# Performance work log

Measured on AMD Instinct MI355X. Metric: run time of the kernel, lower is better.

Reference implementation:

```python
import jax, jax.numpy as jnp
import numpy as np

B, S, E, H, T = 2, 1024, 1024, 16, 32
D = E // H  # head_dim = 64
EPS = 1e-12
SCALE = float(np.sqrt(T) / np.sqrt(D))  # sqrt(num_templates) * 1/sqrt(head_dim)


def _apply_rope(q, k):
    # q, k: [B, S, H, D] float32 (source casts to float for RoPE)
    d = q.shape[-1]
    s = q.shape[1]
    inv_freq = 1.0 / (10000.0 ** (jnp.arange(0, d, 2, dtype=jnp.float32) / d))
    ang = jnp.arange(s, dtype=jnp.float32)[:, None] * inv_freq[None, :]  # [S, D/2]
    cis = jnp.exp(1j * ang)[None, :, None, :]  # [1, S, 1, D/2] complex64

    def rot(v):
        vc = v.reshape(v.shape[:-1] + (d // 2, 2))
        vc = jax.lax.complex(vc[..., 0], vc[..., 1]) * cis
        return jnp.stack([jnp.real(vc), jnp.imag(vc)], axis=-1).reshape(v.shape)

    return rot(q), rot(k)


def _l2norm(v):
    # F.normalize(v, dim=-1): v / max(||v||, eps)
    n = jnp.sqrt(jnp.sum(v * v, axis=-1, keepdims=True))
    return v / jnp.maximum(n, EPS)


def _forward(x, Wq, Wk, Wv, Wo, templates, bind_proj):
    b, s, e = x.shape
    h, d = H, D
    q = (x @ Wq.T).reshape(b, s, h, d)
    k = (x @ Wk.T).reshape(b, s, h, d)
    v = (x @ Wv.T).reshape(b, s, h, d)
    q, k = _apply_rope(q, k)
    q = q.transpose(0, 2, 1, 3)  # [B,H,S,D]
    k = k.transpose(0, 2, 1, 3)
    v = v.transpose(0, 2, 1, 3)

    tpl = _l2norm(templates)  # [H,T,D]
    # forward rfft uses norm='ortho' in the source
    q_freq = jnp.fft.rfft(q, axis=-1, norm='ortho')  # [B,H,S,F], F=D//2+1
    k_freq = jnp.fft.rfft(k, axis=-1, norm='ortho')
    t_conj = jnp.conj(jnp.fft.rfft(tpl, axis=-1, norm='ortho'))[None, :, None, :, :]  # [1,H,1,T,F]

    # NOTE: irfft in the source uses the DEFAULT 'backward' norm (asymmetric with
    # the ortho rfft) -- reproduce that exactly.
    q_bind = jnp.fft.irfft(q_freq[:, :, :, None, :] * t_conj, n=d, axis=-1)  # [B,H,S,T,D]
    k_bind = jnp.fft.irfft(k_freq[:, :, :, None, :] * t_conj, n=d, axis=-1)

    proj = bind_proj[None, :, None, None, :]  # [1,H,1,1,D]
    q_sig = _l2norm(jnp.sum(q_bind * proj, axis=-1))  # [B,H,S,T]
    k_sig = _l2norm(jnp.sum(k_bind * proj, axis=-1))

    scores = jnp.einsum('bhqt,bhkt->bhqk', q_sig, k_sig) * SCALE  # [B,H,S,S]
    attn = jax.nn.softmax(scores, axis=-1)  # dropout is identity in eval mode
    out = jnp.einsum('bhqk,bhkd->bqhd', attn, v).reshape(b, s, e)
    return out @ Wo.T


def setup_inputs() -> dict:
    key = jax.random.key(0)
    ks = jax.random.split(key, 7)
    lim = 1.0 / np.sqrt(E)
    x = jax.random.normal(ks[0], (B, S, E), jnp.float32)
    Wq = jax.random.uniform(ks[1], (E, E), jnp.float32, -lim, lim)
    Wk = jax.random.uniform(ks[2], (E, E), jnp.float32, -lim, lim)
    Wv = jax.random.uniform(ks[3], (E, E), jnp.float32, -lim, lim)
    Wo = jax.random.uniform(ks[4], (E, E), jnp.float32, -lim, lim)
    templates = jax.random.normal(ks[5], (H, T, D), jnp.float32)
    bind_proj = jax.random.normal(ks[6], (H, D), jnp.float32) * 0.02
    return {"x": x, "Wq": Wq, "Wk": Wk, "Wv": Wv, "Wo": Wo,
            "templates": templates, "bind_proj": bind_proj}


def reference(x, Wq, Wk, Wv, Wo, templates, bind_proj):
    return _forward(x, Wq, Wk, Wv, Wo, templates, bind_proj)
```

## Files before the change

kernel.cpp:

```cpp
#include <hip/hip_runtime.h>
#include <math.h>

#define S_ 1024
#define T_ 32
#define SCALE_F 0.7071067811865476f

typedef unsigned int uint;
typedef unsigned short ushort;
typedef __bf16 bf16x8 __attribute__((ext_vector_type(8)));
typedef float f32x16 __attribute__((ext_vector_type(16)));

union FragU { uint4 q; bf16x8 v; };

#define MFMA(a, b, c) __builtin_amdgcn_mfma_f32_32x32x16_bf16((a), (b), (c), 0, 0, 0)

__device__ __forceinline__ uint rne16(float f) {
  uint u = __builtin_bit_cast(uint, f);
  u += 0x7fffu + ((u >> 16) & 1u);
  return u >> 16;
}

__device__ __forceinline__ void split8a(const float* f, uint4& hi, uint4& lo) {
  uint h[8], m[8];
#pragma unroll
  for (int i = 0; i < 8; ++i) {
    uint u = __builtin_bit_cast(uint, f[i]);
    h[i] = u >> 16;
    float fh = __builtin_bit_cast(float, u & 0xffff0000u);
    m[i] = __builtin_bit_cast(uint, f[i] - fh) >> 16;
  }
  hi = make_uint4(h[0] | (h[1] << 16), h[2] | (h[3] << 16),
                  h[4] | (h[5] << 16), h[6] | (h[7] << 16));
  lo = make_uint4(m[0] | (m[1] << 16), m[2] | (m[3] << 16),
                  m[4] | (m[5] << 16), m[6] | (m[7] << 16));
}

__device__ __forceinline__ uint4 rne8(const float4& A, const float4& B) {
  float f[8] = {A.x, A.y, A.z, A.w, B.x, B.y, B.z, B.w};
  uint h[8];
#pragma unroll
  for (int i = 0; i < 8; ++i) h[i] = rne16(f[i]);
  return make_uint4(h[0] | (h[1] << 16), h[2] | (h[3] << 16),
                    h[4] | (h[5] << 16), h[6] | (h[7] << 16));
}

__global__ __launch_bounds__(256) void k_cvtall(
    const float* __restrict__ X, const float* __restrict__ Wq,
    const float* __restrict__ Wk, const float* __restrict__ Wv,
    const float* __restrict__ Wo, ushort* __restrict__ Xb,
    ushort* __restrict__ Wqb, ushort* __restrict__ Wkb,
    ushort* __restrict__ Wvb, ushort* __restrict__ Wob) {
  int i = blockIdx.x * 256 + threadIdx.x;
  const float* src;
  ushort* dst;
  int j;
  if (i < 262144)      { src = X;  dst = Xb;  j = i; }
  else if (i < 393216) { src = Wq; dst = Wqb; j = i - 262144; }
  else if (i < 524288) { src = Wk; dst = Wkb; j = i - 393216; }
  else if (i < 655360) { src = Wv; dst = Wvb; j = i - 524288; }
  else                 { src = Wo; dst = Wob; j = i - 655360; }
  float4 a = *reinterpret_cast<const float4*>(src + j * 8);
  float4 b = *reinterpret_cast<const float4*>(src + j * 8 + 4);
  *reinterpret_cast<uint4*>(dst + j * 8) = rne8(a, b);
}

__global__ __launch_bounds__(64) void k_cs(float* __restrict__ cs) {
  int s = blockIdx.x * 2 + (threadIdx.x >> 5);
  int p = threadIdx.x & 31;
  float invf = powf(10000.0f, (-2.0f * p) / 64.0f);
  float sn, c;
  sincosf((float)s * invf, &sn, &c);
  cs[s * 64 + 2 * p] = c;
  cs[s * 64 + 2 * p + 1] = sn;
}

__global__ __launch_bounds__(64) void k_prep_A(const float* __restrict__ tpl,
                                               const float* __restrict__ proj,
                                               ushort* __restrict__ Ahh,
                                               ushort* __restrict__ Ahl) {
  int ht = blockIdx.x;
  int h = ht >> 5;
  int lane = threadIdx.x;
  float tv = tpl[ht * 64 + lane];
  float ss = tv * tv;
#pragma unroll
  for (int off = 1; off < 64; off <<= 1) ss += __shfl_xor(ss, off);
  float rn = 1.0f / fmaxf(sqrtf(ss), 1e-12f);
  __shared__ float tn[64];
  tn[lane] = tv * rn;
  __syncthreads();
  float acc = 0.f;
#pragma unroll
  for (int j = 0; j < 64; ++j) acc += proj[h * 64 + j] * tn[(lane - j) & 63];
  float v = acc * 0.125f;
  uint u = __builtin_bit_cast(uint, v);
  uint hi = u >> 16;
  float fh = __builtin_bit_cast(float, u & 0xffff0000u);
  uint lo = __builtin_bit_cast(uint, v - fh) >> 16;
  Ahh[ht * 64 + lane] = (ushort)hi;
  Ahl[ht * 64 + lane] = (ushort)lo;
}

__global__ __launch_bounds__(256) void k_qkv(
    const ushort* __restrict__ Xb,
    const ushort* __restrict__ Wqb, const ushort* __restrict__ Wkb,
    const ushort* __restrict__ Wvb,
    const ushort* __restrict__ Ahh, const ushort* __restrict__ Ahl,
    const float* __restrict__ cs,
    ushort* __restrict__ Qs, ushort* __restrict__ Ks,
    ushort* __restrict__ Vt) {
  __shared__ __align__(16) char smem[34816];

  const int z = blockIdx.z;
  const ushort* Wm = (z == 0) ? Wqb : (z == 1) ? Wkb : Wvb;
  const int m0 = blockIdx.y * 128;
  const int n0 = blockIdx.x * 64;
  const int h = blockIdx.x;

  const int tid = threadIdx.x;
  const int l = tid & 63;
  const int wid = tid >> 6;
  const int wr = wid >> 1, wc = wid & 1;
  const int l31 = l & 31, lhi = l >> 5;

  const int sr = tid >> 2;
  const int sc = tid & 3;

  const int offA0 = (sr) * 64 + ((sc ^ ((sr >> 1) & 3)) << 4);
  const int offA1 = (sr + 64) * 64 + ((sc ^ (((sr + 64) >> 1) & 3)) << 4);
  const int offB = 8192 + sr * 64 + ((sc ^ ((sr >> 1) & 3)) << 4);

  const ushort* apsrc0 = Xb + (size_t)(m0 + sr) * 1024 + sc * 8;
  const ushort* apsrc1 = Xb + (size_t)(m0 + sr + 64) * 1024 + sc * 8;
  const ushort* bpsrc = Wm + (size_t)(n0 + sr) * 1024 + sc * 8;

  f32x16 acc0 = 0.0f, acc1 = 0.0f;

  {
    uint4 a0 = *reinterpret_cast<const uint4*>(apsrc0);
    uint4 a1 = *reinterpret_cast<const uint4*>(apsrc1);
    uint4 b = *reinterpret_cast<const uint4*>(bpsrc);
    *reinterpret_cast<uint4*>(smem + offA0) = a0;
    *reinterpret_cast<uint4*>(smem + offA1) = a1;
    *reinterpret_cast<uint4*>(smem + offB) = b;
  }
  __syncthreads();

  int cur = 0;
  for (int t = 0; t < 32; ++t) {
    const bool more = (t < 31);
    uint4 na0, na1, nb;
    if (more) {
      const int kn = (t + 1) * 32;
      na0 = *reinterpret_cast<const uint4*>(apsrc0 + kn);
      na1 = *reinterpret_cast<const uint4*>(apsrc1 + kn);
      nb = *reinterpret_cast<const uint4*>(bpsrc + kn);
    }

    const char* base = smem + cur * 12288;
#pragma unroll
    for (int kst = 0; kst < 2; ++kst) {
      FragU ah0, ah1, bh;
      {
        int row = wr * 64 + l31;
        int cc = (kst * 2 + lhi) ^ ((row >> 1) & 3);
        ah0.q = *reinterpret_cast<const uint4*>(base + row * 64 + cc * 16);
      }
      {
        int row = wr * 64 + 32 + l31;
        int cc = (kst * 2 + lhi) ^ ((row >> 1) & 3);
        ah1.q = *reinterpret_cast<const uint4*>(base + row * 64 + cc * 16);
      }
      {
        int brow = wc * 32 + l31;
        int bcc = (kst * 2 + lhi) ^ ((brow >> 1) & 3);
        bh.q = *reinterpret_cast<const uint4*>(base + 8192 + brow * 64 + bcc * 16);
      }
      acc0 = MFMA(ah0.v, bh.v, acc0);
      acc1 = MFMA(ah1.v, bh.v, acc1);
    }

    if (more) {
      char* dst = smem + (cur ^ 1) * 12288;
      *reinterpret_cast<uint4*>(dst + offA0) = na0;
      *reinterpret_cast<uint4*>(dst + offA1) = na1;
      *reinterpret_cast<uint4*>(dst + offB) = nb;
      __syncthreads();
      cur ^= 1;
    }
  }

  if (z == 2) {
    int d = wc * 32 + l31;
#pragma unroll
    for (int fm = 0; fm < 2; ++fm) {
      const f32x16& a = fm ? acc1 : acc0;
#pragma unroll
      for (int j = 0; j < 16; ++j) {
        int rl = fm * 32 + (j & 3) + ((j >> 2) & 3) * 8 + 4 * lhi;
        int m = m0 + wr * 64 + rl;
        int b = m >> 10, s = m & 1023;
        Vt[((size_t)((b * 16 + h) * 64 + d)) * 1024 + s] = (ushort)rne16(a[j]);
      }
    }
    return;
  }

  ushort* Sig = (z == 0) ? Qs : Ks;
  float* dmp = reinterpret_cast<float*>(smem);
  __syncthreads();
#pragma unroll
  for (int fm = 0; fm < 2; ++fm) {
    const f32x16& a = fm ? acc1 : acc0;
#pragma unroll
    for (int j = 0; j < 16; ++j) {
      int rl = fm * 32 + (j & 3) + ((j >> 2) & 3) * 8 + 4 * lhi;
      dmp[(wr * 64 + rl) * 68 + wc * 32 + l31] = a[j];
    }
  }
  __syncthreads();

  int srow = wr * 64 + wc * 32 + l31;
  int sq = (m0 + srow) & 1023;
  f32x16 sacc = 0.0f;
#pragma unroll
  for (int kst = 0; kst < 4; ++kst) {
    const float* dp = &dmp[srow * 68 + kst * 16 + lhi * 8];
    float4 x0 = *reinterpret_cast<const float4*>(dp);
    float4 x1 = *reinterpret_cast<const float4*>(dp + 4);
    const float* cp = &cs[sq * 64 + kst * 16 + lhi * 8];
    float4 c0 = *reinterpret_cast<const float4*>(cp);
    float4 c1 = *reinterpret_cast<const float4*>(cp + 4);
    float r[8];
    r[0] = x0.x * c0.x - x0.y * c0.y;
    r[1] = x0.x * c0.y + x0.y * c0.x;
    r[2] = x0.z * c0.z - x0.w * c0.w;
    r[3] = x0.z * c0.w + x0.w * c0.z;
    r[4] = x1.x * c1.x - x1.y * c1.y;
    r[5] = x1.x * c1.y + x1.y * c1.x;
    r[6] = x1.z * c1.z - x1.w * c1.w;
    r[7] = x1.z * c1.w + x1.w * c1.z;
    FragU ah, al;
    split8a(r, ah.q, al.q);
    size_t boff = ((size_t)(h * 32 + l31) * 64 + kst * 16 + lhi * 8);
    FragU bh, bl;
    bh.q = *reinterpret_cast<const uint4*>(Ahh + boff);
    bl.q = *reinterpret_cast<const uint4*>(Ahl + boff);
    sacc = MFMA(al.v, bh.v, sacc);
    sacc = MFMA(ah.v, bl.v, sacc);
    sacc = MFMA(ah.v, bh.v, sacc);
  }
#pragma unroll
  for (int j = 0; j < 16; ++j) {
    float v = sacc[j];
    float ss = v * v;
    ss += __shfl_xor(ss, 1);
    ss += __shfl_xor(ss, 2);
    ss += __shfl_xor(ss, 4);
    ss += __shfl_xor(ss, 8);
    ss += __shfl_xor(ss, 16);
    float rn = 1.0f / fmaxf(sqrtf(ss), 1e-12f);
    int rl = (j & 3) + ((j >> 2) & 3) * 8 + 4 * lhi;
    int m = m0 + wr * 64 + wc * 32 + rl;
    int bb = m >> 10, s2 = m & 1023;
    Sig[(((size_t)(bb * 16 + h)) * 1024 + s2) * 32 + l31] =
        (ushort)rne16(v * rn);
  }
}

__global__ __launch_bounds__(128) void k_attn(const ushort* __restrict__ Qs,
                                              const ushort* __restrict__ Ks,
                                              const ushort* __restrict__ Vt,
                                              float* __restrict__ Po,
                                              float* __restrict__ Pd) {
  __shared__ ushort plds[2][32][68];

  const int tid = threadIdx.x;
  const int l = tid & 63;
  const int wid = tid >> 6;
  const int l31 = l & 31, lhi = l >> 5;
  const int bh = blockIdx.y;
  const int z = blockIdx.z;
  const int q0 = blockIdx.x * 64 + wid * 32;

  FragU aq0, aq1;
  {
    const ushort* qp = Qs + ((size_t)bh * 1024 + q0 + l31) * 32 + lhi * 8;
    aq0.q = *reinterpret_cast<const uint4*>(qp);
    aq1.q = *reinterpret_cast<const uint4*>(qp + 16);
  }

  const ushort* kbase = Ks + (size_t)bh * 1024 * 32;
  const ushort* vbase = Vt + (size_t)bh * 64 * 1024;

  f32x16 oacc0 = 0.0f, oacc1 = 0.0f;
  float pden[16];
#pragma unroll
  for (int r = 0; r < 16; ++r) pden[r] = 0.f;

  for (int kt = z * 4; kt < z * 4 + 4; ++kt) {
    const int k0 = kt * 64;
    f32x16 sacc[2];
    sacc[0] = 0.0f;
    sacc[1] = 0.0f;
#pragma unroll
    for (int nt = 0; nt < 2; ++nt) {
      const ushort* kp = kbase + (size_t)(k0 + nt * 32 + l31) * 32 + lhi * 8;
      FragU b0, b1;
      b0.q = *reinterpret_cast<const uint4*>(kp);
      b1.q = *reinterpret_cast<const uint4*>(kp + 16);
      sacc[nt] = MFMA(aq0.v, b0.v, sacc[nt]);
      sacc[nt] = MFMA(aq1.v, b1.v, sacc[nt]);
    }
#pragma unroll
    for (int nt = 0; nt < 2; ++nt) {
#pragma unroll
      for (int r = 0; r < 16; ++r) {
        float e = __expf(sacc[nt][r] * SCALE_F);
        pden[r] += e;
        int q = (r & 3) + ((r >> 2) << 3) + 4 * lhi;
        plds[wid][q][nt * 32 + l31] = (ushort)rne16(e);
      }
    }
    __builtin_amdgcn_wave_barrier();
#pragma unroll
    for (int kst = 0; kst < 4; ++kst) {
      FragU ap;
      const ushort* pp = &plds[wid][l31][kst * 16 + lhi * 8];
      uint2 plo = *reinterpret_cast<const uint2*>(pp);
      uint2 phi = *reinterpret_cast<const uint2*>(pp + 4);
      ap.q = make_uint4(plo.x, plo.y, phi.x, phi.y);
      FragU bv0, bv1;
      const ushort* vp0 = vbase + (size_t)l31 * 1024 + k0 + kst * 16 + lhi * 8;
      bv0.q = *reinterpret_cast<const uint4*>(vp0);
      bv1.q = *reinterpret_cast<const uint4*>(vp0 + 32 * 1024);
      oacc0 = MFMA(ap.v, bv0.v, oacc0);
      oacc1 = MFMA(ap.v, bv1.v, oacc1);
    }
  }

#pragma unroll
  for (int r = 0; r < 16; ++r) {
    float s = pden[r];
    s += __shfl_xor(s, 1);
    s += __shfl_xor(s, 2);
    s += __shfl_xor(s, 4);
    s += __shfl_xor(s, 8);
    s += __shfl_xor(s, 16);
    pden[r] = s;
  }

  const size_t zb = (size_t)z * 32 + bh;
#pragma unroll
  for (int r = 0; r < 16; ++r) {
    int q = q0 + (r & 3) + ((r >> 2) << 3) + 4 * lhi;
    size_t row = zb * 1024 + q;
    Po[row * 64 + l31] = oacc0[r];
    Po[row * 64 + 32 + l31] = oacc1[r];
    if (l31 == 0) Pd[row] = pden[r];
  }
}

__global__ __launch_bounds__(256) void k_attnred(const float* __restrict__ Po,
                                                 const float* __restrict__ Pd,
                                                 ushort* __restrict__ O) {
  int idx = blockIdx.x * 4 + (threadIdx.x >> 6);
  int d = threadIdx.x & 63;
  float den = 0.f, val = 0.f;
#pragma unroll
  for (int zc = 0; zc < 4; ++zc) {
    size_t row = (size_t)zc * 32768 + idx;
    den += Pd[row];
    val += Po[row * 64 + d];
  }
  int bh = idx >> 10, q = idx & 1023;
  int b = bh >> 4, h = bh & 15;
  O[((size_t)(b * 1024 + q)) * 1024 + h * 64 + d] = (ushort)rne16(val / den);
}

__global__ __launch_bounds__(128) void k_attn_mono(const ushort* __restrict__ Qs,
                                                   const ushort* __restrict__ Ks,
                                                   const ushort* __restrict__ Vt,
                                                   ushort* __restrict__ O) {
  __shared__ ushort plds[2][32][68];

  const int tid = threadIdx.x;
  const int l = tid & 63;
  const int wid = tid >> 6;
  const int l31 = l & 31, lhi = l >> 5;
  const int bh = blockIdx.y;
  const int q0 = blockIdx.x * 64 + wid * 32;

  FragU aq0, aq1;
  {
    const ushort* qp = Qs + ((size_t)bh * 1024 + q0 + l31) * 32 + lhi * 8;
    aq0.q = *reinterpret_cast<const uint4*>(qp);
    aq1.q = *reinterpret_cast<const uint4*>(qp + 16);
  }

  const ushort* kbase = Ks + (size_t)bh * 1024 * 32;
  const ushort* vbase = Vt + (size_t)bh * 64 * 1024;

  f32x16 oacc0 = 0.0f, oacc1 = 0.0f;
  float pden[16];
#pragma unroll
  for (int r = 0; r < 16; ++r) pden[r] = 0.f;

  for (int kt = 0; kt < 16; ++kt) {
    const int k0 = kt * 64;
    f32x16 sacc[2];
    sacc[0] = 0.0f;
    sacc[1] = 0.0f;
#pragma unroll
    for (int nt = 0; nt < 2; ++nt) {
      const ushort* kp = kbase + (size_t)(k0 + nt * 32 + l31) * 32 + lhi * 8;
      FragU b0, b1;
      b0.q = *reinterpret_cast<const uint4*>(kp);
      b1.q = *reinterpret_cast<const uint4*>(kp + 16);
      sacc[nt] = MFMA(aq0.v, b0.v, sacc[nt]);
      sacc[nt] = MFMA(aq1.v, b1.v, sacc[nt]);
    }
#pragma unroll
    for (int nt = 0; nt < 2; ++nt) {
#pragma unroll
      for (int r = 0; r < 16; ++r) {
        float e = __expf(sacc[nt][r] * SCALE_F);
        pden[r] += e;
        int q = (r & 3) + ((r >> 2) << 3) + 4 * lhi;
        plds[wid][q][nt * 32 + l31] = (ushort)rne16(e);
      }
    }
    __builtin_amdgcn_wave_barrier();
#pragma unroll
    for (int kst = 0; kst < 4; ++kst) {
      FragU ap;
      const ushort* pp = &plds[wid][l31][kst * 16 + lhi * 8];
      uint2 plo = *reinterpret_cast<const uint2*>(pp);
      uint2 phi = *reinterpret_cast<const uint2*>(pp + 4);
      ap.q = make_uint4(plo.x, plo.y, phi.x, phi.y);
      FragU bv0, bv1;
      const ushort* vp0 = vbase + (size_t)l31 * 1024 + k0 + kst * 16 + lhi * 8;
      bv0.q = *reinterpret_cast<const uint4*>(vp0);
      bv1.q = *reinterpret_cast<const uint4*>(vp0 + 32 * 1024);
      oacc0 = MFMA(ap.v, bv0.v, oacc0);
      oacc1 = MFMA(ap.v, bv1.v, oacc1);
    }
  }

#pragma unroll
  for (int r = 0; r < 16; ++r) {
    float s = pden[r];
    s += __shfl_xor(s, 1);
    s += __shfl_xor(s, 2);
    s += __shfl_xor(s, 4);
    s += __shfl_xor(s, 8);
    s += __shfl_xor(s, 16);
    pden[r] = 1.0f / s;
  }

  const int b = bh >> 4, h = bh & 15;
#pragma unroll
  for (int r = 0; r < 16; ++r) {
    int q = q0 + (r & 3) + ((r >> 2) << 3) + 4 * lhi;
    size_t row = ((size_t)b * 1024 + q) * 1024 + h * 64;
    O[row + l31] = (ushort)rne16(oacc0[r] * pden[r]);
    O[row + 32 + l31] = (ushort)rne16(oacc1[r] * pden[r]);
  }
}

__global__ __launch_bounds__(256) void k_final(const ushort* __restrict__ Xb,
                                               const ushort* __restrict__ Wb,
                                               float* __restrict__ Y) {
  __shared__ __align__(16) char smem[16384];

  const int m0 = blockIdx.y * 64;
  const int n0 = blockIdx.x * 64;
  const int tid = threadIdx.x;
  const int l = tid & 63;
  const int wid = tid >> 6;
  const int wr = wid >> 1, wc = wid & 1;
  const int l31 = l & 31, lhi = l >> 5;
  const int sr = tid >> 2;
  const int sc = tid & 3;

  const int offA = sr * 64 + ((sc ^ ((sr >> 1) & 3)) << 4);
  const int offB = 4096 + offA;
  const ushort* apsrc = Xb + (size_t)(m0 + sr) * 1024 + sc * 8;
  const ushort* bpsrc = Wb + (size_t)(n0 + sr) * 1024 + sc * 8;

  f32x16 acc = 0.0f;

  {
    uint4 av = *reinterpret_cast<const uint4*>(apsrc);
    uint4 bv = *reinterpret_cast<const uint4*>(bpsrc);
    *reinterpret_cast<uint4*>(smem + offA) = av;
    *reinterpret_cast<uint4*>(smem + offB) = bv;
  }
  __syncthreads();

  int cur = 0;
  for (int t = 0; t < 32; ++t) {
    const bool more = (t < 31);
    uint4 na, nb;
    if (more) {
      const int kn = (t + 1) * 32;
      na = *reinterpret_cast<const uint4*>(apsrc + kn);
      nb = *reinterpret_cast<const uint4*>(bpsrc + kn);
    }

    const char* base = smem + cur * 8192;
#pragma unroll
    for (int kst = 0; kst < 2; ++kst) {
      FragU ah, bh;
      int row = wr * 32 + l31;
      int cc = (kst * 2 + lhi) ^ ((row >> 1) & 3);
      ah.q = *reinterpret_cast<const uint4*>(base + row * 64 + cc * 16);
      int brow = wc * 32 + l31;
      int bcc = (kst * 2 + lhi) ^ ((brow >> 1) & 3);
      bh.q = *reinterpret_cast<const uint4*>(base + 4096 + brow * 64 + bcc * 16);
      acc = MFMA(ah.v, bh.v, acc);
    }

    if (more) {
      char* dst = smem + (cur ^ 1) * 8192;
      *reinterpret_cast<uint4*>(dst + offA) = na;
      *reinterpret_cast<uint4*>(dst + offB) = nb;
      __syncthreads();
      cur ^= 1;
    }
  }

#pragma unroll
  for (int j = 0; j < 16; ++j) {
    int rl = (j & 3) + ((j >> 2) & 3) * 8 + 4 * lhi;
    int m = m0 + wr * 32 + rl;
    Y[(size_t)m * 1024 + n0 + wc * 32 + l31] = acc[j];
  }
}

extern "C" void kernel_launch(void* const* d_in, const int* in_sizes, int n_in,
                              void* d_out, int out_size, void* d_ws,
                              size_t ws_size, hipStream_t stream) {
  const float* x = (const float*)d_in[0];
  const float* Wq = (const float*)d_in[1];
  const float* Wk = (const float*)d_in[2];
  const float* Wv = (const float*)d_in[3];
  const float* Wo = (const float*)d_in[4];
  const float* tpl = (const float*)d_in[5];
  const float* proj = (const float*)d_in[6];
  float* out = (float*)d_out;

  char* ws = (char*)d_ws;
  size_t off = 0;
  auto alloc = [&](size_t bytes) {
    void* p = ws + off;
    off += (bytes + 255) & ~(size_t)255;
    return p;
  };

  const size_t MB = 1024 * 1024;
  bool huge = ws_size >= 64 * MB;
  bool big = ws_size >= 22 * MB;

  ushort *Xb, *Wvb, *obuf;
  float* cs;
  ushort *Ahh, *Ahl, *Wqb, *Wkb, *Wob, *qs, *ks, *vt;
  float *Po = nullptr, *Pd = nullptr;

  if (big || huge) {
    Xb = (ushort*)alloc(4 * MB);
    cs = (float*)alloc((size_t)1024 * 64 * 4);
    Ahh = (ushort*)alloc((size_t)16 * 32 * 64 * 2);
    Ahl = (ushort*)alloc((size_t)16 * 32 * 64 * 2);
    Wqb = (ushort*)alloc(2 * MB);
    Wkb = (ushort*)alloc(2 * MB);
    Wvb = (ushort*)alloc(2 * MB);
    Wob = (ushort*)alloc(2 * MB);
    qs = (ushort*)alloc(2 * MB);
    ks = (ushort*)alloc(2 * MB);
    vt = (ushort*)alloc(4 * MB);
    if (huge) {
      Po = (float*)alloc(32 * MB);
      Pd = (float*)alloc((size_t)4 * 32768 * 4);
    }
    obuf = Xb;
  } else {
    cs = (float*)alloc((size_t)1024 * 64 * 4);
    Ahh = (ushort*)alloc((size_t)16 * 32 * 64 * 2);
    Ahl = (ushort*)alloc((size_t)16 * 32 * 64 * 2);
    Wqb = (ushort*)alloc(2 * MB);
    Wkb = (ushort*)alloc(2 * MB);
    Wob = (ushort*)alloc(2 * MB);
    qs = (ushort*)alloc(2 * MB);
    ks = (ushort*)alloc(2 * MB);
    vt = (ushort*)alloc(4 * MB);
    obuf = (ushort*)ws;
    Xb = (ushort*)d_out;
    Wvb = (ushort*)((char*)d_out + 4 * MB);
  }

  k_cvtall<<<dim3(3072), dim3(256), 0, stream>>>(x, Wq, Wk, Wv, Wo, Xb, Wqb,
                                                 Wkb, Wvb, Wob);
  k_cs<<<dim3(512), dim3(64), 0, stream>>>(cs);
  k_prep_A<<<dim3(512), dim3(64), 0, stream>>>(tpl, proj, Ahh, Ahl);
  k_qkv<<<dim3(16, 16, 3), dim3(256), 0, stream>>>(Xb, Wqb, Wkb, Wvb, Ahh, Ahl,
                                                   cs, qs, ks, vt);
  if (huge) {
    k_attn<<<dim3(16, 32, 4), dim3(128), 0, stream>>>(qs, ks, vt, Po, Pd);
    k_attnred<<<dim3(8192), dim3(256), 0, stream>>>(Po, Pd, obuf);
  } else {
    k_attn_mono<<<dim3(16, 32), dim3(128), 0, stream>>>(qs, ks, vt, obuf);
  }
  k_final<<<dim3(16, 32), dim3(256), 0, stream>>>(obuf, Wob, out);
}
```

Measured before the change: 95.47 us.

## Deepen GEMM global prefetch to two stages and store attention partials in bf16

Both GEMM kernels now hold one extra k-tile in registers, loading two tiles ahead of the shared-memory stage. This gives global loads more time to land before they are needed, at the cost of extra registers. The split-K attention partial outputs are also written as bf16 instead of fp32, which halves the traffic for the partial write and the reduction read. The bf16 partials add rounding error before the final normalisation.

```diff
diff --git a/kernel.cpp b/kernel.cpp
--- a/kernel.cpp
+++ b/kernel.cpp
@@ -18,6 +18,10 @@
   uint u = __builtin_bit_cast(uint, f);
   u += 0x7fffu + ((u >> 16) & 1u);
   return u >> 16;
+}
+
+__device__ __forceinline__ float bf2f(ushort u) {
+  return __builtin_bit_cast(float, ((uint)u) << 16);
 }
 
 __device__ __forceinline__ void split8a(const float* f, uint4& hi, uint4& lo) {
@@ -137,21 +141,24 @@
   f32x16 acc0 = 0.0f, acc1 = 0.0f;
 
   {
-    uint4 a0 = *reinterpret_cast<const uint4*>(apsrc0);
-    uint4 a1 = *reinterpret_cast<const uint4*>(apsrc1);
-    uint4 b = *reinterpret_cast<const uint4*>(bpsrc);
-    *reinterpret_cast<uint4*>(smem + offA0) = a0;
-    *reinterpret_cast<uint4*>(smem + offA1) = a1;
-    *reinterpret_cast<uint4*>(smem + offB) = b;
-  }
+    *reinterpret_cast<uint4*>(smem + offA0) =
+        *reinterpret_cast<const uint4*>(apsrc0);
+    *reinterpret_cast<uint4*>(smem + offA1) =
+        *reinterpret_cast<const uint4*>(apsrc1);
+    *reinterpret_cast<uint4*>(smem + offB) =
+        *reinterpret_cast<const uint4*>(bpsrc);
+  }
+  uint4 ra0 = *reinterpret_cast<const uint4*>(apsrc0 + 32);
+  uint4 ra1 = *reinterpret_cast<const uint4*>(apsrc1 + 32);
+  uint4 rb = *reinterpret_cast<const uint4*>(bpsrc + 32);
   __syncthreads();
 
   int cur = 0;
+#pragma unroll 4
   for (int t = 0; t < 32; ++t) {
-    const bool more = (t < 31);
     uint4 na0, na1, nb;
-    if (more) {
-      const int kn = (t + 1) * 32;
+    if (t < 30) {
+      const int kn = (t + 2) * 32;
       na0 = *reinterpret_cast<const uint4*>(apsrc0 + kn);
       na1 = *reinterpret_cast<const uint4*>(apsrc1 + kn);
       nb = *reinterpret_cast<const uint4*>(bpsrc + kn);
@@ -180,13 +187,14 @@
       acc1 = MFMA(ah1.v, bh.v, acc1);
     }
 
-    if (more) {
+    if (t < 31) {
       char* dst = smem + (cur ^ 1) * 12288;
-      *reinterpret_cast<uint4*>(dst + offA0) = na0;
-      *reinterpret_cast<uint4*>(dst + offA1) = na1;
-      *reinterpret_cast<uint4*>(dst + offB) = nb;
+      *reinterpret_cast<uint4*>(dst + offA0) = ra0;
+      *reinterpret_cast<uint4*>(dst + offA1) = ra1;
+      *reinterpret_cast<uint4*>(dst + offB) = rb;
       __syncthreads();
       cur ^= 1;
+      if (t < 30) { ra0 = na0; ra1 = na1; rb = nb; }
     }
   }
 
@@ -271,7 +279,7 @@
 __global__ __launch_bounds__(128) void k_attn(const ushort* __restrict__ Qs,
                                               const ushort* __restrict__ Ks,
                                               const ushort* __restrict__ Vt,
-                                              float* __restrict__ Po,
+                                              ushort* __restrict__ Po,
                                               float* __restrict__ Pd) {
   __shared__ ushort plds[2][32][68];
 
@@ -355,13 +363,13 @@
   for (int r = 0; r < 16; ++r) {
     int q = q0 + (r & 3) + ((r >> 2) << 3) + 4 * lhi;
     size_t row = zb * 1024 + q;
-    Po[row * 64 + l31] = oacc0[r];
-    Po[row * 64 + 32 + l31] = oacc1[r];
+    Po[row * 64 + l31] = (ushort)rne16(oacc0[r]);
+    Po[row * 64 + 32 + l31] = (ushort)rne16(oacc1[r]);
     if (l31 == 0) Pd[row] = pden[r];
   }
 }
 
-__global__ __launch_bounds__(256) void k_attnred(const float* __restrict__ Po,
+__global__ __launch_bounds__(256) void k_attnred(const ushort* __restrict__ Po,
                                                  const float* __restrict__ Pd,
                                                  ushort* __restrict__ O) {
   int idx = blockIdx.x * 4 + (threadIdx.x >> 6);
@@ -371,7 +379,7 @@
   for (int zc = 0; zc < 4; ++zc) {
     size_t row = (size_t)zc * 32768 + idx;
     den += Pd[row];
-    val += Po[row * 64 + d];
+    val += bf2f(Po[row * 64 + d]);
   }
   int bh = idx >> 10, q = idx & 1023;
   int b = bh >> 4, h = bh & 15;
@@ -491,19 +499,21 @@
   f32x16 acc = 0.0f;
 
   {
-    uint4 av = *reinterpret_cast<const uint4*>(apsrc);
-    uint4 bv = *reinterpret_cast<const uint4*>(bpsrc);
-    *reinterpret_cast<uint4*>(smem + offA) = av;
-    *reinterpret_cast<uint4*>(smem + offB) = bv;
-  }
+    *reinterpret_cast<uint4*>(smem + offA) =
+        *reinterpret_cast<const uint4*>(apsrc);
+    *reinterpret_cast<uint4*>(smem + offB) =
+        *reinterpret_cast<const uint4*>(bpsrc);
+  }
+  uint4 ra = *reinterpret_cast<const uint4*>(apsrc + 32);
+  uint4 rb = *reinterpret_cast<const uint4*>(bpsrc + 32);
   __syncthreads();
 
   int cur = 0;
+#pragma unroll 4
   for (int t = 0; t < 32; ++t) {
-    const bool more = (t < 31);
     uint4 na, nb;
-    if (more) {
-      const int kn = (t + 1) * 32;
+    if (t < 30) {
+      const int kn = (t + 2) * 32;
       na = *reinterpret_cast<const uint4*>(apsrc + kn);
       nb = *reinterpret_cast<const uint4*>(bpsrc + kn);
     }
@@ -521,12 +531,13 @@
       acc = MFMA(ah.v, bh.v, acc);
     }
 
-    if (more) {
+    if (t < 31) {
       char* dst = smem + (cur ^ 1) * 8192;
-      *reinterpret_cast<uint4*>(dst + offA) = na;
-      *reinterpret_cast<uint4*>(dst + offB) = nb;
+      *reinterpret_cast<uint4*>(dst + offA) = ra;
+      *reinterpret_cast<uint4*>(dst + offB) = rb;
       __syncthreads();
       cur ^= 1;
+      if (t < 30) { ra = na; rb = nb; }
     }
   }
 
@@ -565,7 +576,8 @@
   ushort *Xb, *Wvb, *obuf;
   float* cs;
   ushort *Ahh, *Ahl, *Wqb, *Wkb, *Wob, *qs, *ks, *vt;
-  float *Po = nullptr, *Pd = nullptr;
+  ushort* Po = nullptr;
+  float* Pd = nullptr;
 
   if (big || huge) {
     Xb = (ushort*)alloc(4 * MB);
@@ -580,7 +592,7 @@
     ks = (ushort*)alloc(2 * MB);
     vt = (ushort*)alloc(4 * MB);
     if (huge) {
-      Po = (float*)alloc(32 * MB);
+      Po = (ushort*)alloc(16 * MB);
       Pd = (float*)alloc((size_t)4 * 32768 * 4);
     }
     obuf = Xb;
```

Measured after the change: 90.71 us. 5.0% less time.
